# Kernel tuning notes

Measured on AMD Instinct MI355X. Metric: run time of the kernel, lower is better.

## Reference

```python
import jax, jax.numpy as jnp
import numpy as np

N = 50000        # num nodes
E = 800000       # num edges (avg degree 16)
IN = 64          # in_channels
H = 128          # hidden_channels
C1 = 64          # Num_TCN (fine clusters)
C2 = 16          # Num_TCN2 (coarse clusters)
DROP = 0.5       # drop_rate
THRESH = 1.0 / (C1 - 1)  # default edge_pruning_threshold
LN_EPS = 1e-5


def layer_norm(x, g, b):
    mu = jnp.mean(x, axis=-1, keepdims=True)
    var = jnp.var(x, axis=-1, keepdims=True)
    return (x - mu) * jax.lax.rsqrt(var + LN_EPS) * g + b


def graph_conv(x_src, row, col, W_rel, b, W_root, num_nodes):
    # PyG GraphConv (aggr='add'): out = lin_rel(sum_{src->dst} x[src]) + lin_root(x)
    agg = jax.ops.segment_sum(x_src[row], col, num_segments=num_nodes)
    return agg @ W_rel.T + b + x_src @ W_root.T


def mincut_common(x, s, A_s, deg):
    # shared tail of sparse_mincut_pool given A_s = A @ s and degree vector
    C = s.shape[-1]
    pooled_x = s.T @ x                                   # [C, F]
    pooled_adj = s.T @ A_s                               # [C, C]
    mincut_num = jnp.trace(pooled_adj)
    mincut_den = jnp.trace(s.T @ (deg[:, None] * s)) + 1e-10
    mincut_loss = -mincut_num / mincut_den
    sTs = s.T @ s
    norm = jnp.linalg.norm(sTs)
    ortho_loss = jnp.linalg.norm(sTs / (norm + 1e-10) - jnp.eye(C, dtype=x.dtype) / jnp.sqrt(jnp.asarray(C, x.dtype)))
    adj = pooled_adj * (1.0 - jnp.eye(C, dtype=x.dtype))  # fill_diagonal_(0)
    d_sqrt_inv = 1.0 / (jnp.sqrt(adj.sum(axis=1)) + 1e-15)
    adj_norm = adj * d_sqrt_inv[:, None] * d_sqrt_inv[None, :]
    return pooled_x, adj_norm, mincut_loss, ortho_loss


def mincut_sparse(x, row, col, s_logits, num_nodes):
    s = jax.nn.softmax(s_logits, axis=-1)
    # A_s[row] += s[col]  (edge_weight = 1) -> [N, C] scatter-add
    A_s = jax.ops.segment_sum(s[col], row, num_segments=num_nodes)
    deg = jax.ops.segment_sum(jnp.ones((row.shape[0],), x.dtype), row, num_segments=num_nodes)
    return mincut_common(x, s, A_s, deg)


def mincut_dense(x, M, s_logits):
    # pooled graph: dense 0/1 adjacency M[i,j]; equivalent to edge list from nonzero(M)
    s = jax.nn.softmax(s_logits, axis=-1)
    A_s = M @ s
    deg = M.sum(axis=1)
    return mincut_common(x, s, A_s, deg)


def setup_inputs() -> dict:
    key = jax.random.key(0)
    ks = jax.random.split(key, 12)
    x = jax.random.normal(ks[0], (N, IN), jnp.float32)
    edge_index = jax.random.randint(ks[1], (2, E), 0, N, jnp.int32)
    # bernoulli(1 - drop_rate) node-drop mask, fixed for determinism
    drop_mask = (jax.random.uniform(ks[2], (N,)) > DROP).astype(jnp.float32)
    p = lambda k, shp: (jax.random.normal(k, shp, jnp.float32) * 0.05)
    return dict(
        x=x, edge_index=edge_index, drop_mask=drop_mask,
        W1_rel=p(ks[3], (H, IN)), b1=jnp.zeros((H,), jnp.float32), W1_root=p(ks[4], (H, IN)),
        pW1=p(ks[5], (C1, H)), pb1=jnp.zeros((C1,), jnp.float32),
        g1=jnp.ones((C1,), jnp.float32), be1=jnp.zeros((C1,), jnp.float32),
        W2_rel=p(ks[6], (H, H)), b2=jnp.zeros((H,), jnp.float32), W2_root=p(ks[7], (H, H)),
        pW2=p(ks[8], (C2, H)), pb2=jnp.zeros((C2,), jnp.float32),
        g2=jnp.ones((C2,), jnp.float32), be2=jnp.zeros((C2,), jnp.float32),
    )


def reference(x, edge_index, drop_mask, W1_rel, b1, W1_root, pW1, pb1, g1, be1,
              W2_rel, b2, W2_root, pW2, pb2, g2, be2):
    # training=True path, S=1 (loss sums / S are identity)
    row, col = edge_index[0], edge_index[1]
    x_drop = drop_mask[:, None] * x
    x1 = jax.nn.relu(graph_conv(x_drop, row, col, W1_rel, b1, W1_root, N))   # [N, H]
    s1 = layer_norm(x1 @ pW1.T + pb1, g1, be1)                               # [N, C1]
    ls1 = jax.nn.log_softmax(s1, axis=-1)
    x_pool1, adj_pool1, mc1, o1 = mincut_sparse(x1, row, col, s1, N)
    # edge pruning -> dense 0/1 pooled adjacency (replaces nonzero + edge list)
    M = jnp.where(adj_pool1 > THRESH, 1.0, 0.0).astype(x.dtype)              # [C1, C1]
    # GraphConv on pooled graph: aggregate x[src] at dst == M.T @ x_pool1
    x2 = jax.nn.relu((M.T @ x_pool1) @ W2_rel.T + b2 + x_pool1 @ W2_root.T)  # [C1, H]
    s2 = layer_norm(x2 @ pW2.T + pb2, g2, be2)                               # [C1, C2]
    ls2 = jax.nn.log_softmax(s2, axis=-1)
    _, _, mc2, o2 = mincut_dense(x2, M, s2)
    return (mc1, o1, mc2, o2, ls1, ls2)
```

## Files before the change

kernel.cpp:

```cpp
#include <hip/hip_runtime.h>
#include <hip/hip_bf16.h>

#define NN 50000
#define NE 800000
#define INC 64
#define HC 128
#define NC1 64
#define NC2 16
#define DCAP 64

#define OFF_FLAG 0
#define OFW_W1R 16
#define OFW_W1O 8208
#define OFW_B1  16400
#define OFW_PW1 16528
#define OFW_PB1 24720
#define OFW_G1  24784
#define OFW_BE1 24848
#define OFW_W2R 24912
#define OFW_B2  41296
#define OFW_W2O 41424
#define OFW_PW2 57808
#define OFW_PB2 59856
#define OFW_G2  59872
#define OFW_BE2 59888
#define CVT_TOTAL 59888

#define OFW_PW1T 59904
#define OFF_MG   68096
#define OFF_MTG  72192
#define OFF_DEG2 76288
#define OFF_S2G  76352
#define OFW_WCT  77376
#define OFF_XD   127792
#define OFF_X1   3327792
#define OFF_S    9727792
#define OFF_AGG  12927792
#define OFF_CSRC 16127792
#define OFF_SCAL 17727792
#define OFF_PX   17727808
#define OFF_PADJ 17736000
#define OFF_STS  17740096
#define OFF_CUR  17744192
#define OFF_Q    17794192
#define OFF_END  17844192
#define ZERO_FLOATS (OFF_END - OFF_SCAL)

#define OFF_PXSTSP OFF_XD
#define OFF_PADJP  OFF_X1
#define P_POOL 256
#define P_PADJ 1024
#define XSS 132

__device__ inline float bflo(unsigned int u){ return __uint_as_float(u << 16); }
__device__ inline float bfhi(unsigned int u){ return __uint_as_float(u & 0xffff0000u); }

__device__ inline float wave_sum(float v){
#pragma unroll
  for (int o = 32; o > 0; o >>= 1) v += __shfl_xor(v, o, 64);
  return v;
}

__device__ inline void store_out(void* out, long long idx, float v, bool bf){
  if (bf) ((__hip_bfloat16*)out)[idx] = __float2bfloat16(v);
  else    ((float*)out)[idx] = v;
}

__device__ inline float block_reduce_256(float v, float* red, int t){
  red[t] = v; __syncthreads();
#pragma unroll
  for (int sh = 128; sh > 0; sh >>= 1){
    if (t < sh) red[t] += red[t + sh];
    __syncthreads();
  }
  float r = red[0];
  __syncthreads();
  return r;
}

__global__ void k_detect(const unsigned int* __restrict__ dmw, float* __restrict__ flag){
  __shared__ int cnt;
  if (threadIdx.x == 0) cnt = 0;
  __syncthreads();
  int c = 0;
  for (int i = threadIdx.x; i < 12288; i += 256){
    unsigned int w = dmw[i];
    if (w == 0x3F803F80u || w == 0x00003F80u) c++;
  }
  atomicAdd(&cnt, c);
  __syncthreads();
  if (threadIdx.x == 0) flag[0] = (cnt > 64) ? 1.0f : 0.0f;
}

__global__ void k_cvt(const void* p0, const void* p1, const void* p2, const void* p3,
                      const void* p4, const void* p5, const void* p6, const void* p7,
                      const void* p8, const void* p9, const void* p10, const void* p11,
                      const void* p12, const void* p13,
                      const float* __restrict__ flag, float* __restrict__ ws){
  int i = blockIdx.x * blockDim.x + threadIdx.x;
  if (i >= CVT_TOTAL) return;
  const void* src; int off;
  if      (i < 8192 ){ src = p0;  off = i; }
  else if (i < 16384){ src = p1;  off = i - 8192; }
  else if (i < 16512){ src = p2;  off = i - 16384; }
  else if (i < 24704){ src = p3;  off = i - 16512; }
  else if (i < 24768){ src = p4;  off = i - 24704; }
  else if (i < 24832){ src = p5;  off = i - 24768; }
  else if (i < 24896){ src = p6;  off = i - 24832; }
  else if (i < 41280){ src = p7;  off = i - 24896; }
  else if (i < 41408){ src = p8;  off = i - 41280; }
  else if (i < 57792){ src = p9;  off = i - 41408; }
  else if (i < 59840){ src = p10; off = i - 57792; }
  else if (i < 59856){ src = p11; off = i - 59840; }
  else if (i < 59872){ src = p12; off = i - 59856; }
  else               { src = p13; off = i - 59872; }
  float v = (flag[0] > 0.5f) ? __bfloat162float(((const __hip_bfloat16*)src)[off])
                             : ((const float*)src)[off];
  ws[16 + i] = v;
  if (i < 8192){
    int h = i >> 6, j = i & 63;
    ws[OFW_WCT + j * 128 + h] = v;
  } else if (i < 16384){
    int o2 = i - 8192;
    int h = o2 >> 6, j = o2 & 63;
    ws[OFW_WCT + (64 + j) * 128 + h] = v;
  } else if (i >= 16512 && i < 24704){
    int o2 = i - 16512;
    int c = o2 >> 7, k = o2 & 127;
    ws[OFW_PW1T + k * 64 + c] = v;
  }
}

__global__ void k_xdrop(const void* __restrict__ xr, const void* __restrict__ dmr,
                        const float* __restrict__ flag, float* __restrict__ xd){
  int i4 = blockIdx.x * blockDim.x + threadIdx.x;
  if (i4 >= NN * 16) return;
  int n = i4 >> 4;
  float4 o;
  if (flag[0] > 0.5f){
    uint2 w = ((const uint2*)xr)[i4];
    float dv = __bfloat162float(((const __hip_bfloat16*)dmr)[n]);
    o.x = bflo(w.x) * dv; o.y = bfhi(w.x) * dv;
    o.z = bflo(w.y) * dv; o.w = bfhi(w.y) * dv;
  } else {
    float4 xv = ((const float4*)xr)[i4];
    float dv = ((const float*)dmr)[n];
    o.x = xv.x * dv; o.y = xv.y * dv; o.z = xv.z * dv; o.w = xv.w * dv;
  }
  ((float4*)xd)[i4] = o;
}

__global__ void k_fillC(const int* __restrict__ ei, int* __restrict__ cur,
                        unsigned short* __restrict__ csrc2){
  int e = blockIdx.x * blockDim.x + threadIdx.x;
  if (e < NE){
    int r = ei[e], c = ei[NE + e];
    int pos = atomicAdd(&cur[c], 1);
    if (pos < DCAP) csrc2[(c << 6) + pos] = (unsigned short)r;
  }
}

__device__ inline float4 gather_rowsum16(const unsigned short* __restrict__ idxarr,
                                         int st, int en,
                                         const float* __restrict__ table, int lane,
                                         int g, int sub){
  float4 a0 = {0,0,0,0}, a1 = {0,0,0,0}, a2 = {0,0,0,0}, a3 = {0,0,0,0};
  for (int bb = st; bb < en; bb += 64){
    int rem = en - bb;
    int myi = (bb + lane < en) ? (int)idxarr[bb + lane] : 0;
    int niter = ((rem < 64 ? rem : 64) + 3) >> 2;
    int i = 0;
    for (; i + 4 <= niter; i += 4){
      int s0 = __shfl(myi, g + ((i    ) << 2), 64);
      int s1 = __shfl(myi, g + ((i + 1) << 2), 64);
      int s2 = __shfl(myi, g + ((i + 2) << 2), 64);
      int s3 = __shfl(myi, g + ((i + 3) << 2), 64);
      if ((g + (i << 2))       < rem){ float4 v = *(const float4*)(table + (s0 << 6) + (sub << 2)); a0.x += v.x; a0.y += v.y; a0.z += v.z; a0.w += v.w; }
      if ((g + ((i + 1) << 2)) < rem){ float4 v = *(const float4*)(table + (s1 << 6) + (sub << 2)); a1.x += v.x; a1.y += v.y; a1.z += v.z; a1.w += v.w; }
      if ((g + ((i + 2) << 2)) < rem){ float4 v = *(const float4*)(table + (s2 << 6) + (sub << 2)); a2.x += v.x; a2.y += v.y; a2.z += v.z; a2.w += v.w; }
      if ((g + ((i + 3) << 2)) < rem){ float4 v = *(const float4*)(table + (s3 << 6) + (sub << 2)); a3.x += v.x; a3.y += v.y; a3.z += v.z; a3.w += v.w; }
    }
    for (; i < niter; ++i){
      int slot = g + (i << 2);
      int s0 = __shfl(myi, slot, 64);
      if (slot < rem){ float4 v = *(const float4*)(table + (s0 << 6) + (sub << 2)); a0.x += v.x; a0.y += v.y; a0.z += v.z; a0.w += v.w; }
    }
  }
  float4 a;
  a.x = (a0.x + a1.x) + (a2.x + a3.x);
  a.y = (a0.y + a1.y) + (a2.y + a3.y);
  a.z = (a0.z + a1.z) + (a2.z + a3.z);
  a.w = (a0.w + a1.w) + (a2.w + a3.w);
  a.x += __shfl_xor(a.x, 16, 64); a.x += __shfl_xor(a.x, 32, 64);
  a.y += __shfl_xor(a.y, 16, 64); a.y += __shfl_xor(a.y, 32, 64);
  a.z += __shfl_xor(a.z, 16, 64); a.z += __shfl_xor(a.z, 32, 64);
  a.w += __shfl_xor(a.w, 16, 64); a.w += __shfl_xor(a.w, 32, 64);
  return a;
}

__global__ __launch_bounds__(256) void k_agg2(const int* __restrict__ cur,
                                              const unsigned short* __restrict__ csrc2,
                                              const float* __restrict__ xd,
                                              float* __restrict__ agg){
  int gid = blockIdx.x * 256 + threadIdx.x;
  int lane = gid & 63, wid = gid >> 6;
  int nw = (gridDim.x * 256) >> 6;
  int g = lane >> 4, sub = lane & 15;
  for (int n = wid; n < NN; n += nw){
    int c = cur[n]; if (c > DCAP) c = DCAP;
    int st = n << 6, en = st + c;
    float4 a = gather_rowsum16(csrc2, st, en, xd, lane, g, sub);
    if (g == 0) *(float4*)(agg + (n << 6) + (sub << 2)) = a;
  }
}

#define FMA4(ACC, AV) \
  ACC.x += AV.x*w0.x + AV.y*w1.x + AV.z*w2.x + AV.w*w3.x; \
  ACC.y += AV.x*w0.y + AV.y*w1.y + AV.z*w2.y + AV.w*w3.y; \
  ACC.z += AV.x*w0.z + AV.y*w1.z + AV.z*w2.z + AV.w*w3.z; \
  ACC.w += AV.x*w0.w + AV.y*w1.w + AV.z*w2.w + AV.w*w3.w;

__global__ __launch_bounds__(512, 2) void k_x1(const float* __restrict__ agg,
                                               const float* __restrict__ xd,
                                               const float* __restrict__ wts,
                                               float* __restrict__ x1){
  __shared__ __align__(16) float wt[128 * 128];
  __shared__ __align__(16) float at[64 * 128];
  int t = threadIdx.x;
  for (int f4 = t; f4 < 4096; f4 += 512)
    *(float4*)&wt[f4 << 2] = *(const float4*)&wts[OFW_WCT + (f4 << 2)];
  int ni = t >> 5;
  int cj = t & 31;
  float4 b4 = *(const float4*)&wts[OFW_B1 + (cj << 2)];
  const int ntiles = (NN + 63) >> 6;
  for (int tile = blockIdx.x; tile < ntiles; tile += gridDim.x){
    int base = tile << 6;
    __syncthreads();
    for (int f4 = t; f4 < 2048; f4 += 512){
      int i = f4 >> 5, kq = f4 & 31;
      int n = base + i;
      float4 v = make_float4(0.f, 0.f, 0.f, 0.f);
      if (n < NN){
        int k = kq << 2;
        v = (k < 64) ? *(const float4*)(agg + (n << 6) + k)
                     : *(const float4*)(xd  + (n << 6) + (k - 64));
      }
      *(float4*)&at[(i << 7) + (kq << 2)] = v;
    }
    __syncthreads();
    float4 acc0 = {0,0,0,0}, acc1 = {0,0,0,0}, acc2 = {0,0,0,0}, acc3 = {0,0,0,0};
    const float* ap = at + (ni << 9);
    const float* wp = wt + (cj << 2);
#pragma unroll 4
    for (int k = 0; k < 128; k += 4){
      float4 w0 = *(const float4*)(wp + ((k + 0) << 7));
      float4 w1 = *(const float4*)(wp + ((k + 1) << 7));
      float4 w2 = *(const float4*)(wp + ((k + 2) << 7));
      float4 w3 = *(const float4*)(wp + ((k + 3) << 7));
      float4 a0v = *(const float4*)(ap + k);
      float4 a1v = *(const float4*)(ap + 128 + k);
      float4 a2v = *(const float4*)(ap + 256 + k);
      float4 a3v = *(const float4*)(ap + 384 + k);
      FMA4(acc0, a0v)
      FMA4(acc1, a1v)
      FMA4(acc2, a2v)
      FMA4(acc3, a3v)
    }
    int n0 = base + (ni << 2);
    if (n0 + 0 < NN){
      float4 o; o.x = fmaxf(acc0.x + b4.x, 0.f); o.y = fmaxf(acc0.y + b4.y, 0.f);
      o.z = fmaxf(acc0.z + b4.z, 0.f); o.w = fmaxf(acc0.w + b4.w, 0.f);
      *(float4*)(x1 + (long long)(n0 + 0) * HC + (cj << 2)) = o;
    }
    if (n0 + 1 < NN){
      float4 o; o.x = fmaxf(acc1.x + b4.x, 0.f); o.y = fmaxf(acc1.y + b4.y, 0.f);
      o.z = fmaxf(acc1.z + b4.z, 0.f); o.w = fmaxf(acc1.w + b4.w, 0.f);
      *(float4*)(x1 + (long long)(n0 + 1) * HC + (cj << 2)) = o;
    }
    if (n0 + 2 < NN){
      float4 o; o.x = fmaxf(acc2.x + b4.x, 0.f); o.y = fmaxf(acc2.y + b4.y, 0.f);
      o.z = fmaxf(acc2.z + b4.z, 0.f); o.w = fmaxf(acc2.w + b4.w, 0.f);
      *(float4*)(x1 + (long long)(n0 + 2) * HC + (cj << 2)) = o;
    }
    if (n0 + 3 < NN){
      float4 o; o.x = fmaxf(acc3.x + b4.x, 0.f); o.y = fmaxf(acc3.y + b4.y, 0.f);
      o.z = fmaxf(acc3.z + b4.z, 0.f); o.w = fmaxf(acc3.w + b4.w, 0.f);
      *(float4*)(x1 + (long long)(n0 + 3) * HC + (cj << 2)) = o;
    }
  }
}

__global__ __launch_bounds__(256) void k_s1f(const float* __restrict__ x1,
                                             const float* __restrict__ wts,
                                             float* __restrict__ s,
                                             float* __restrict__ q,
                                             void* __restrict__ outp,
                                             const float* __restrict__ flag){
  __shared__ float xs[64 * XSS];
  __shared__ float pwc[64 * 64];
  __shared__ float gsh[64], bsh[64];
  int t = threadIdx.x;
  int base = blockIdx.x * 64;
  if (t < 64){ gsh[t] = wts[OFW_G1 + t]; bsh[t] = wts[OFW_BE1 + t]; }
  for (int f = t; f < 64 * 32; f += 256){
    int r = f >> 5, kq = f & 31;
    float4 v = (base + r < NN) ? *(const float4*)(x1 + (base + r) * HC + (kq << 2))
                               : make_float4(0, 0, 0, 0);
    *(float4*)&xs[r * XSS + (kq << 2)] = v;
  }
  int ni = t >> 4, cj = t & 15;
  float4 c0 = {0,0,0,0}, c1 = {0,0,0,0}, c2 = {0,0,0,0}, c3 = {0,0,0,0};
#pragma unroll
  for (int half = 0; half < 2; ++half){
    int k0 = half << 6;
    __syncthreads();
    for (int f = t; f < 1024; f += 256){
      int kk = f >> 4, qq = f & 15;
      *(float4*)&pwc[kk * 64 + (qq << 2)] =
          *(const float4*)&wts[OFW_PW1T + (k0 + kk) * 64 + (qq << 2)];
    }
    __syncthreads();
    for (int kk = 0; kk < 64; kk += 4){
      float4 a0 = *(const float4*)&xs[(ni * 4 + 0) * XSS + k0 + kk];
      float4 a1 = *(const float4*)&xs[(ni * 4 + 1) * XSS + k0 + kk];
      float4 a2 = *(const float4*)&xs[(ni * 4 + 2) * XSS + k0 + kk];
      float4 a3 = *(const float4*)&xs[(ni * 4 + 3) * XSS + k0 + kk];
      float4 b0 = *(const float4*)&pwc[(kk + 0) * 64 + (cj << 2)];
      float4 b1 = *(const float4*)&pwc[(kk + 1) * 64 + (cj << 2)];
      float4 b2 = *(const float4*)&pwc[(kk + 2) * 64 + (cj << 2)];
      float4 b3 = *(const float4*)&pwc[(kk + 3) * 64 + (cj << 2)];
      c0.x += a0.x*b0.x + a0.y*b1.x + a0.z*b2.x + a0.w*b3.x;
      c0.y += a0.x*b0.y + a0.y*b1.y + a0.z*b2.y + a0.w*b3.y;
      c0.z += a0.x*b0.z + a0.y*b1.z + a0.z*b2.z + a0.w*b3.z;
      c0.w += a0.x*b0.w + a0.y*b1.w + a0.z*b2.w + a0.w*b3.w;
      c1.x += a1.x*b0.x + a1.y*b1.x + a1.z*b2.x + a1.w*b3.x;
      c1.y += a1.x*b0.y + a1.y*b1.y + a1.z*b2.y + a1.w*b3.y;
      c1.z += a1.x*b0.z + a1.y*b1.z + a1.z*b2.z + a1.w*b3.z;
      c1.w += a1.x*b0.w + a1.y*b1.w + a1.z*b2.w + a1.w*b3.w;
      c2.x += a2.x*b0.x + a2.y*b1.x + a2.z*b2.x + a2.w*b3.x;
      c2.y += a2.x*b0.y + a2.y*b1.y + a2.z*b2.y + a2.w*b3.y;
      c2.z += a2.x*b0.z + a2.y*b1.z + a2.z*b2.z + a2.w*b3.z;
      c2.w += a2.x*b0.w + a2.y*b1.w + a2.z*b2.w + a2.w*b3.w;
      c3.x += a3.x*b0.x + a3.y*b1.x + a3.z*b2.x + a3.w*b3.x;
      c3.y += a3.x*b0.y + a3.y*b1.y + a3.z*b2.y + a3.w*b3.y;
      c3.z += a3.x*b0.z + a3.y*b1.z + a3.z*b2.z + a3.w*b3.z;
      c3.w += a3.x*b0.w + a3.y*b1.w + a3.z*b2.w + a3.w*b3.w;
    }
  }
  float4 pb = *(const float4*)&wts[OFW_PB1 + (cj << 2)];
  c0.x += pb.x; c0.y += pb.y; c0.z += pb.z; c0.w += pb.w;
  c1.x += pb.x; c1.y += pb.y; c1.z += pb.z; c1.w += pb.w;
  c2.x += pb.x; c2.y += pb.y; c2.z += pb.z; c2.w += pb.w;
  c3.x += pb.x; c3.y += pb.y; c3.z += pb.z; c3.w += pb.w;
  __syncthreads();
  *(float4*)&xs[(ni * 4 + 0) * XSS + (cj << 2)] = c0;
  *(float4*)&xs[(ni * 4 + 1) * XSS + (cj << 2)] = c1;
  *(float4*)&xs[(ni * 4 + 2) * XSS + (cj << 2)] = c2;
  *(float4*)&xs[(ni * 4 + 3) * XSS + (cj << 2)] = c3;
  __syncthreads();
  bool bf = flag[0] > 0.5f;
  int lane = t & 63, wv = t >> 6;
  float gl = gsh[lane], bl = bsh[lane];
  for (int rb = 0; rb < 16; rb += 4){
    int row = wv * 16 + rb;
    float z0 = xs[(row + 0) * XSS + lane];
    float z1 = xs[(row + 1) * XSS + lane];
    float z2 = xs[(row + 2) * XSS + lane];
    float z3 = xs[(row + 3) * XSS + lane];
    float s0 = z0, s1 = z1, s2 = z2, s3 = z3;
    float q0 = z0*z0, q1 = z1*z1, q2 = z2*z2, q3 = z3*z3;
#pragma unroll
    for (int o = 32; o > 0; o >>= 1){
      s0 += __shfl_xor(s0, o, 64); q0 += __shfl_xor(q0, o, 64);
      s1 += __shfl_xor(s1, o, 64); q1 += __shfl_xor(q1, o, 64);
      s2 += __shfl_xor(s2, o, 64); q2 += __shfl_xor(q2, o, 64);
      s3 += __shfl_xor(s3, o, 64); q3 += __shfl_xor(q3, o, 64);
    }
    float mu0 = s0 * 0.015625f, mu1 = s1 * 0.015625f;
    float mu2 = s2 * 0.015625f, mu3 = s3 * 0.015625f;
    float va0 = q0 * 0.015625f - mu0 * mu0;
    float va1 = q1 * 0.015625f - mu1 * mu1;
    float va2 = q2 * 0.015625f - mu2 * mu2;
    float va3 = q3 * 0.015625f - mu3 * mu3;
    float y0 = (z0 - mu0) * rsqrtf(va0 + 1e-5f) * gl + bl;
    float y1 = (z1 - mu1) * rsqrtf(va1 + 1e-5f) * gl + bl;
    float y2 = (z2 - mu2) * rsqrtf(va2 + 1e-5f) * gl + bl;
    float y3 = (z3 - mu3) * rsqrtf(va3 + 1e-5f) * gl + bl;
    float m0 = y0, m1 = y1, m2 = y2, m3 = y3;
#pragma unroll
    for (int o = 32; o > 0; o >>= 1){
      m0 = fmaxf(m0, __shfl_xor(m0, o, 64));
      m1 = fmaxf(m1, __shfl_xor(m1, o, 64));
      m2 = fmaxf(m2, __shfl_xor(m2, o, 64));
      m3 = fmaxf(m3, __shfl_xor(m3, o, 64));
    }
    float e0 = expf(y0 - m0), e1 = expf(y1 - m1);
    float e2 = expf(y2 - m2), e3 = expf(y3 - m3);
    float u0 = e0, u1 = e1, u2 = e2, u3 = e3;
    float w0 = e0*e0, w1 = e1*e1, w2 = e2*e2, w3 = e3*e3;
#pragma unroll
    for (int o = 32; o > 0; o >>= 1){
      u0 += __shfl_xor(u0, o, 64); w0 += __shfl_xor(w0, o, 64);
      u1 += __shfl_xor(u1, o, 64); w1 += __shfl_xor(w1, o, 64);
      u2 += __shfl_xor(u2, o, 64); w2 += __shfl_xor(w2, o, 64);
      u3 += __shfl_xor(u3, o, 64); w3 += __shfl_xor(w3, o, 64);
    }
    int n0 = base + row;
    if (n0 + 0 < NN){ s[(n0 + 0) * 64 + lane] = e0 / u0;
      store_out(outp, 4LL + (long long)(n0 + 0) * 64 + lane, (y0 - m0) - logf(u0), bf);
      if (lane == 0) q[n0 + 0] = w0 / (u0 * u0); }
    if (n0 + 1 < NN){ s[(n0 + 1) * 64 + lane] = e1 / u1;
      store_out(outp, 4LL + (long long)(n0 + 1) * 64 + lane, (y1 - m1) - logf(u1), bf);
      if (lane == 0) q[n0 + 1] = w1 / (u1 * u1); }
    if (n0 + 2 < NN){ s[(n0 + 2) * 64 + lane] = e2 / u2;
      store_out(outp, 4LL + (long long)(n0 + 2) * 64 + lane, (y2 - m2) - logf(u2), bf);
      if (lane == 0) q[n0 + 2] = w2 / (u2 * u2); }
    if (n0 + 3 < NN){ s[(n0 + 3) * 64 + lane] = e3 / u3;
      store_out(outp, 4LL + (long long)(n0 + 3) * 64 + lane, (y3 - m3) - logf(u3), bf);
      if (lane == 0) q[n0 + 3] = w3 / (u3 * u3); }
  }
}

__global__ __launch_bounds__(256) void k_den(const int* __restrict__ ei,
                                             const float* __restrict__ q,
                                             float* __restrict__ scal){
  __shared__ float red[256];
  int t = threadIdx.x;
  float acc = 0.0f;
  for (int e = blockIdx.x * 256 + t; e < NE; e += gridDim.x * 256)
    acc += q[ei[e]];
  float r = block_reduce_256(acc, red, t);
  if (t == 0) atomicAdd(&scal[0], r);
}

__global__ __launch_bounds__(256) void k_padj2(const int* __restrict__ cur,
                                               const unsigned short* __restrict__ csrc2,
                                               const float* __restrict__ s,
                                               float* __restrict__ padjp){
  __shared__ float rs[16 * 64];
  __shared__ float ra[16 * 64];
  int t = threadIdx.x, lane = t & 63, w = t >> 6;
  int g = lane >> 4, sub = lane & 15;
  int i4 = t >> 4;
  int j4 = t & 15;
  float4 acc0 = {0,0,0,0}, acc1 = {0,0,0,0}, acc2 = {0,0,0,0}, acc3 = {0,0,0,0};
  const int nbatch = NN / 16;
  for (int b = blockIdx.x; b < nbatch; b += gridDim.x){
    int base = b * 16;
#pragma unroll
    for (int qq = 0; qq < 4; ++qq){
      int k = w * 4 + qq;
      int n = base + k;
      int c = cur[n]; if (c > DCAP) c = DCAP;
      int st = n << 6, en = st + c;
      float4 a = gather_rowsum16(csrc2, st, en, s, lane, g, sub);
      if (g == 0){
        *(float4*)&rs[k * 64 + (sub << 2)] = a;
      } else if (g == 1){
        *(float4*)&ra[k * 64 + (sub << 2)] = *(const float4*)(s + (n << 6) + (sub << 2));
      }
    }
    __syncthreads();
#pragma unroll
    for (int k = 0; k < 16; ++k){
      float4 a  = *(const float4*)&rs[k * 64 + (i4 << 2)];
      float4 bv = *(const float4*)&ra[k * 64 + (j4 << 2)];
      acc0.x += a.x * bv.x; acc0.y += a.x * bv.y; acc0.z += a.x * bv.z; acc0.w += a.x * bv.w;
      acc1.x += a.y * bv.x; acc1.y += a.y * bv.y; acc1.z += a.y * bv.z; acc1.w += a.y * bv.w;
      acc2.x += a.z * bv.x; acc2.y += a.z * bv.y; acc2.z += a.z * bv.z; acc2.w += a.z * bv.w;
      acc3.x += a.w * bv.x; acc3.y += a.w * bv.y; acc3.z += a.w * bv.z; acc3.w += a.w * bv.w;
    }
    __syncthreads();
  }
  float* pp = padjp + blockIdx.x * 4096;
  *(float4*)&pp[(i4 * 4 + 0) * 64 + (j4 << 2)] = acc0;
  *(float4*)&pp[(i4 * 4 + 1) * 64 + (j4 << 2)] = acc1;
  *(float4*)&pp[(i4 * 4 + 2) * 64 + (j4 << 2)] = acc2;
  *(float4*)&pp[(i4 * 4 + 3) * 64 + (j4 << 2)] = acc3;
}

__global__ __launch_bounds__(1024) void k_pool(const float* __restrict__ s,
                                               const float* __restrict__ x1,
                                               float* __restrict__ part){
  __shared__ float ssh[32 * 64];
  __shared__ float xsh[32 * 128];
  int t = threadIdx.x;
  int c = t >> 4, q = t & 15;
  float4 apx0 = {0,0,0,0}, apx1 = {0,0,0,0}, ast0 = {0,0,0,0};
  const int nbatch = (NN + 31) / 32;
  for (int b = blockIdx.x; b < nbatch; b += gridDim.x){
    int base = b * 32;
    int kmax = NN - base; if (kmax > 32) kmax = 32;
    if (t < 512){
      int k = t >> 4, col = t & 15;
      float4 v = (k < kmax) ? *(const float4*)(s + ((base + k) << 6) + (col << 2))
                            : make_float4(0, 0, 0, 0);
      *(float4*)&ssh[k * 64 + (col << 2)] = v;
    }
    {
      int k = t >> 5, col = t & 31;
      float4 v = (k < kmax) ? *(const float4*)(x1 + (base + k) * HC + (col << 2))
                            : make_float4(0, 0, 0, 0);
      *(float4*)&xsh[k * 128 + (col << 2)] = v;
    }
    __syncthreads();
    for (int k = 0; k < kmax; ++k){
      float sv = ssh[k * 64 + c];
      float4 xv0 = *(const float4*)&xsh[k * 128 + (q << 2)];
      float4 xv1 = *(const float4*)&xsh[k * 128 + ((q + 16) << 2)];
      float4 s0  = *(const float4*)&ssh[k * 64 + (q << 2)];
      apx0.x += sv * xv0.x; apx0.y += sv * xv0.y; apx0.z += sv * xv0.z; apx0.w += sv * xv0.w;
      apx1.x += sv * xv1.x; apx1.y += sv * xv1.y; apx1.z += sv * xv1.z; apx1.w += sv * xv1.w;
      ast0.x += sv * s0.x;  ast0.y += sv * s0.y;  ast0.z += sv * s0.z;  ast0.w += sv * s0.w;
    }
    __syncthreads();
  }
  float* pp = part + blockIdx.x * 12288;
  *(float4*)&pp[c * 128 + (q << 2)]        = apx0;
  *(float4*)&pp[c * 128 + ((q + 16) << 2)] = apx1;
  *(float4*)&pp[8192 + c * 64 + (q << 2)]  = ast0;
}

__global__ __launch_bounds__(256) void k_red(const float* __restrict__ pxstsp,
                                             const float* __restrict__ padjp,
                                             float* __restrict__ px,
                                             float* __restrict__ sts,
                                             float* __restrict__ padj){
  __shared__ float sh[256];
  int b = blockIdx.x, t = threadIdx.x;
  int ci = t & 63, pc = t >> 6;
  if (b < 192){
    int cell = b * 64 + ci;
    float a0 = 0, a1 = 0, a2 = 0, a3 = 0;
    const float* basep = pxstsp + cell;
    int p0 = pc * (P_POOL / 4);
    for (int p = 0; p < P_POOL / 4; p += 4){
      a0 += basep[(p0 + p    ) * 12288];
      a1 += basep[(p0 + p + 1) * 12288];
      a2 += basep[(p0 + p + 2) * 12288];
      a3 += basep[(p0 + p + 3) * 12288];
    }
    sh[t] = (a0 + a1) + (a2 + a3);
    __syncthreads();
    if (t < 64){
      float r = sh[t] + sh[t + 64] + sh[t + 128] + sh[t + 192];
      int cell2 = b * 64 + t;
      if (cell2 < 8192) px[cell2] = r; else sts[cell2 - 8192] = r;
    }
  } else {
    int cell = (b - 192) * 64 + ci;
    float a0 = 0, a1 = 0, a2 = 0, a3 = 0;
    const float* basep = padjp + cell;
    int p0 = pc * (P_PADJ / 4);
    for (int p = 0; p < P_PADJ / 4; p += 4){
      a0 += basep[(p0 + p    ) * 4096];
      a1 += basep[(p0 + p + 1) * 4096];
      a2 += basep[(p0 + p + 2) * 4096];
      a3 += basep[(p0 + p + 3) * 4096];
    }
    sh[t] = (a0 + a1) + (a2 + a3);
    __syncthreads();
    if (t < 64) padj[(b - 192) * 64 + t] = sh[t] + sh[t + 64] + sh[t + 128] + sh[t + 192];
  }
}

__global__ __launch_bounds__(256) void k_m(const float* __restrict__ padj,
                                           const float* __restrict__ sts,
                                           float* __restrict__ Mg,
                                           float* __restrict__ Mtg,
                                           float* __restrict__ deg2,
                                           float* __restrict__ scal){
  __shared__ float red[256];
  __shared__ float psh[4096];
  __shared__ float dsi[64];
  int t = threadIdx.x;
  const float TH = 1.0f / 63.0f;
  for (int i = t; i < 4096; i += 256) psh[i] = padj[i];
  __syncthreads();
  float v = (t < 64) ? psh[t * 65] : 0.0f;
  float num1 = block_reduce_256(v, red, t);
  v = 0.0f;
  for (int i = t; i < 4096; i += 256){ float e = sts[i]; v += e * e; }
  float nrm1 = sqrtf(block_reduce_256(v, red, t));
  v = 0.0f;
  for (int i = t; i < 4096; i += 256){
    float e = sts[i] / (nrm1 + 1e-10f) - ((i % 65 == 0) ? 0.125f : 0.0f);
    v += e * e;
  }
  float o1 = sqrtf(block_reduce_256(v, red, t));
  if (t < 64){
    float rs = 0.0f;
    for (int j = 0; j < 64; ++j) rs += (j == t) ? 0.0f : psh[t * 64 + j];
    dsi[t] = 1.0f / (sqrtf(rs) + 1e-15f);
  }
  __syncthreads();
  for (int i = t; i < 4096; i += 256){
    int r = i >> 6, c = i & 63;
    float a = (r == c) ? 0.0f : psh[i];
    float m = (a * dsi[r] * dsi[c] > TH) ? 1.0f : 0.0f;
    Mg[i] = m;
    Mtg[c * 64 + r] = m;
  }
  __syncthreads();
  for (int i = t; i < 4096; i += 256){
    int r = i >> 6, c = i & 63;
    float a = (r == c) ? 0.0f : psh[i];
    psh[i] = (a * dsi[r] * dsi[c] > TH) ? 1.0f : 0.0f;
  }
  __syncthreads();
  if (t < 64){
    float d2 = 0.0f;
    for (int j = 0; j < 64; ++j) d2 += psh[t * 64 + j];
    deg2[t] = d2;
  }
  if (t == 0){ scal[1] = num1; scal[2] = o1; }
}

__global__ __launch_bounds__(128) void k_x2(const float* __restrict__ Mtg,
                                            const float* __restrict__ px,
                                            const float* __restrict__ wts,
                                            float* __restrict__ s2g,
                                            void* __restrict__ out,
                                            const float* __restrict__ flag){
  __shared__ float mt[64], pxc[128], mpsh[128], x2sh[128];
  __shared__ float part[16][9], lsh[16], stat[2];
  int c = blockIdx.x, t = threadIdx.x;
  if (t < 64) mt[t] = Mtg[c * 64 + t];
  pxc[t] = px[c * 128 + t];
  __syncthreads();
  float mp = 0.0f;
  for (int i = 0; i < 64; ++i) mp += mt[i] * px[i * 128 + t];
  mpsh[t] = mp;
  __syncthreads();
  float acc = wts[OFW_B2 + t];
  const float* wrr = wts + OFW_W2R + t * 128;
  const float* wor = wts + OFW_W2O + t * 128;
  for (int k = 0; k < 128; ++k) acc += mpsh[k] * wrr[k] + pxc[k] * wor[k];
  x2sh[t] = fmaxf(acc, 0.0f);
  __syncthreads();
  { int u = t >> 3, p = t & 7;
    const float* pw = wts + OFW_PW2 + u * 128 + p * 16;
    float pa = 0.0f;
    for (int k = 0; k < 16; ++k) pa += x2sh[p * 16 + k] * pw[k];
    part[u][p] = pa;
  }
  __syncthreads();
  if (t < 16){
    float l = wts[OFW_PB2 + t];
    for (int p = 0; p < 8; ++p) l += part[t][p];
    lsh[t] = l;
  }
  __syncthreads();
  if (t == 0){
    float mu = 0.0f;
    for (int u = 0; u < 16; ++u) mu += lsh[u];
    mu *= (1.0f / 16.0f);
    float var = 0.0f;
    for (int u = 0; u < 16; ++u){ float d = lsh[u] - mu; var += d * d; }
    var *= (1.0f / 16.0f);
    float rstd = rsqrtf(var + 1e-5f);
    float m = -3.4e38f;
    for (int u = 0; u < 16; ++u){
      lsh[u] = (lsh[u] - mu) * rstd * wts[OFW_G2 + u] + wts[OFW_BE2 + u];
      m = fmaxf(m, lsh[u]);
    }
    float se = 0.0f;
    for (int u = 0; u < 16; ++u) se += expf(lsh[u] - m);
    stat[0] = m; stat[1] = logf(se);
  }
  __syncthreads();
  if (t < 16){
    float ls = (lsh[t] - stat[0]) - stat[1];
    store_out(out, 4LL + (long long)NN * NC1 + c * 16 + t, ls, flag[0] > 0.5f);
    s2g[c * 16 + t] = expf(ls);
  }
}

__global__ __launch_bounds__(256) void k_tail(const float* __restrict__ Mg,
                                              const float* __restrict__ s2g,
                                              const float* __restrict__ deg2,
                                              const float* __restrict__ scal,
                                              void* __restrict__ out,
                                              const float* __restrict__ flag){
  __shared__ float red[256];
  __shared__ float Msh[4096];
  __shared__ float s2sh[1024];
  __shared__ float d2sh[64];
  __shared__ float sts2[256];
  int t = threadIdx.x;
  for (int i = t; i < 4096; i += 256) Msh[i] = Mg[i];
  for (int i = t; i < 1024; i += 256) s2sh[i] = s2g[i];
  if (t < 64) d2sh[t] = deg2[t];
  __syncthreads();
  float vnum = 0.0f, vden = 0.0f;
  for (int m = 0; m < 4; ++m){
    int id = t + m * 256;
    int c = id >> 4, u = id & 15;
    float a = 0.0f;
    for (int j = 0; j < 64; ++j) a += Msh[c * 64 + j] * s2sh[j * 16 + u];
    float sv = s2sh[id];
    vnum += sv * a;
    vden += d2sh[c] * sv * sv;
  }
  float num2 = block_reduce_256(vnum, red, t);
  float den2 = block_reduce_256(vden, red, t) + 1e-10f;
  { int u = t >> 4, w = t & 15;
    float a = 0.0f;
    for (int c2 = 0; c2 < 64; ++c2) a += s2sh[c2 * 16 + u] * s2sh[c2 * 16 + w];
    sts2[t] = a;
  }
  __syncthreads();
  float v = sts2[t] * sts2[t];
  float nrm2 = sqrtf(block_reduce_256(v, red, t));
  { float e = sts2[t] / (nrm2 + 1e-10f) - (((t >> 4) == (t & 15)) ? 0.25f : 0.0f);
    v = e * e; }
  float o2 = sqrtf(block_reduce_256(v, red, t));
  if (t == 0){
    bool bf = flag[0] > 0.5f;
    float den = scal[0] + 1e-10f;
    store_out(out, 0, -scal[1] / den, bf);
    store_out(out, 1, scal[2], bf);
    store_out(out, 2, -num2 / den2, bf);
    store_out(out, 3, o2, bf);
  }
}

extern "C" void kernel_launch(void* const* d_in, const int* in_sizes, int n_in,
                              void* d_out, int out_size, void* d_ws, size_t ws_size,
                              hipStream_t stream){
  const void* x  = d_in[0];
  const int*  ei = (const int*)d_in[1];
  const void* dm = d_in[2];

  float* ws    = (float*)d_ws;
  float* flag  = ws + OFF_FLAG;
  float* xd    = ws + OFF_XD;
  float* x1    = ws + OFF_X1;
  float* s     = ws + OFF_S;
  float* agg   = ws + OFF_AGG;
  float* px    = ws + OFF_PX;
  float* padj  = ws + OFF_PADJ;
  float* sts   = ws + OFF_STS;
  float* scal  = ws + OFF_SCAL;
  float* Mg    = ws + OFF_MG;
  float* Mtg   = ws + OFF_MTG;
  float* deg2  = ws + OFF_DEG2;
  float* s2g   = ws + OFF_S2G;
  float* q     = ws + OFF_Q;
  float* pxstsp= ws + OFF_PXSTSP;
  float* padjp = ws + OFF_PADJP;
  unsigned short* csrc2 = (unsigned short*)(ws + OFF_CSRC);
  int* cur = (int*)(ws + OFF_CUR);

  hipMemsetAsync(ws + OFF_SCAL, 0, (size_t)ZERO_FLOATS * sizeof(float), stream);

  k_detect<<<1, 256, 0, stream>>>((const unsigned int*)dm, flag);
  k_cvt<<<(CVT_TOTAL + 255) / 256, 256, 0, stream>>>(
      d_in[3], d_in[5], d_in[4], d_in[6], d_in[7], d_in[8], d_in[9],
      d_in[10], d_in[11], d_in[12], d_in[13], d_in[14], d_in[15], d_in[16],
      flag, ws);
  k_xdrop<<<(NN * 16 + 255) / 256, 256, 0, stream>>>(x, dm, flag, xd);
  k_fillC<<<(NE + 255) / 256, 256, 0, stream>>>(ei, cur, csrc2);
  k_agg2<<<2048, 256, 0, stream>>>(cur, csrc2, xd, agg);
  k_x1<<<256, 512, 0, stream>>>(agg, xd, ws, x1);
  k_s1f<<<(NN + 63) / 64, 256, 0, stream>>>(x1, ws, s, q, d_out, flag);
  k_den<<<256, 256, 0, stream>>>(ei, q, scal);
  k_pool<<<P_POOL, 1024, 0, stream>>>(s, x1, pxstsp);
  k_padj2<<<P_PADJ, 256, 0, stream>>>(cur, csrc2, s, padjp);
  k_red<<<256, 256, 0, stream>>>(pxstsp, padjp, px, sts, padj);
  k_m<<<1, 256, 0, stream>>>(padj, sts, Mg, Mtg, deg2, scal);
  k_x2<<<64, 128, 0, stream>>>(Mtg, px, ws, s2g, d_out, flag);
  k_tail<<<1, 256, 0, stream>>>(Mg, s2g, deg2, scal, d_out, flag);
}
```

Baseline: 435.9 us.

## Gather aggregation from fp16 feature copy and partition CSR fill by destination range

The dropped-input features are also written as an fp16 copy into the x1 workspace region, and the neighbor-sum gather reads this half-width table and accumulates in fp32, halving the random gather traffic. The edge bucketing kernel now splits edges into slices, and each slice is scanned by 8 blocks that each handle only destinations in one eighth of the node range. This is meant to localise atomics and stores by destination. The trade-off is that every block re-reads the destination indices of its slice, and the fp16 rounding of inputs adds precision loss to the aggregation. The fp16 buffer aliases x1, which is written later, so reuse relies on kernel ordering.

```diff
diff --git a/kernel.cpp b/kernel.cpp
--- a/kernel.cpp
+++ b/kernel.cpp
@@ -1,5 +1,6 @@
 #include <hip/hip_runtime.h>
 #include <hip/hip_bf16.h>
+#include <hip/hip_fp16.h>
 
 #define NN 50000
 #define NE 800000
@@ -48,9 +49,15 @@
 
 #define OFF_PXSTSP OFF_XD
 #define OFF_PADJP  OFF_X1
+#define OFF_XD16   OFF_X1
 #define P_POOL 256
 #define P_PADJ 1024
 #define XSS 132
+
+#define FC_G 2048
+#define FC_SLICES (FC_G >> 3)
+#define FC_ES ((NE + FC_SLICES - 1) / FC_SLICES)
+#define FC_RANGE (NN >> 3)
 
 __device__ inline float bflo(unsigned int u){ return __uint_as_float(u << 16); }
 __device__ inline float bfhi(unsigned int u){ return __uint_as_float(u & 0xffff0000u); }
@@ -132,7 +139,8 @@
 }
 
 __global__ void k_xdrop(const void* __restrict__ xr, const void* __restrict__ dmr,
-                        const float* __restrict__ flag, float* __restrict__ xd){
+                        const float* __restrict__ flag, float* __restrict__ xd,
+                        __half* __restrict__ xd16){
   int i4 = blockIdx.x * blockDim.x + threadIdx.x;
   if (i4 >= NN * 16) return;
   int n = i4 >> 4;
@@ -148,15 +156,28 @@
     o.x = xv.x * dv; o.y = xv.y * dv; o.z = xv.z * dv; o.w = xv.w * dv;
   }
   ((float4*)xd)[i4] = o;
-}
-
-__global__ void k_fillC(const int* __restrict__ ei, int* __restrict__ cur,
+  __half2 ha = __floats2half2_rn(o.x, o.y);
+  __half2 hb = __floats2half2_rn(o.z, o.w);
+  uint2 hh;
+  hh.x = *(unsigned int*)&ha;
+  hh.y = *(unsigned int*)&hb;
+  ((uint2*)xd16)[i4] = hh;
+}
+
+__global__ __launch_bounds__(256) void k_fillC(const int* __restrict__ ei, int* __restrict__ cur,
                         unsigned short* __restrict__ csrc2){
-  int e = blockIdx.x * blockDim.x + threadIdx.x;
-  if (e < NE){
-    int r = ei[e], c = ei[NE + e];
-    int pos = atomicAdd(&cur[c], 1);
-    if (pos < DCAP) csrc2[(c << 6) + pos] = (unsigned short)r;
+  int p = blockIdx.x & 7;
+  int q = blockIdx.x >> 3;
+  int lo = p * FC_RANGE;
+  int base = q * FC_ES;
+  int end = base + FC_ES; if (end > NE) end = NE;
+  for (int e = base + (int)threadIdx.x; e < end; e += 256){
+    int c = ei[NE + e];
+    if ((unsigned)(c - lo) < (unsigned)FC_RANGE){
+      int r = ei[e];
+      int pos = atomicAdd(&cur[c], 1);
+      if (pos < DCAP) csrc2[(c << 6) + pos] = (unsigned short)r;
+    }
   }
 }
 
@@ -198,9 +219,67 @@
   return a;
 }
 
+__device__ inline float4 gather_rowsum16h(const unsigned short* __restrict__ idxarr,
+                                          int st, int en,
+                                          const __half* __restrict__ table, int lane,
+                                          int g, int sub){
+  float4 a0 = {0,0,0,0}, a1 = {0,0,0,0}, a2 = {0,0,0,0}, a3 = {0,0,0,0};
+  for (int bb = st; bb < en; bb += 64){
+    int rem = en - bb;
+    int myi = (bb + lane < en) ? (int)idxarr[bb + lane] : 0;
+    int niter = ((rem < 64 ? rem : 64) + 3) >> 2;
+    int i = 0;
+    for (; i + 4 <= niter; i += 4){
+      int s0 = __shfl(myi, g + ((i    ) << 2), 64);
+      int s1 = __shfl(myi, g + ((i + 1) << 2), 64);
+      int s2 = __shfl(myi, g + ((i + 2) << 2), 64);
+      int s3 = __shfl(myi, g + ((i + 3) << 2), 64);
+      if ((g + (i << 2))       < rem){
+        uint2 u = *(const uint2*)(table + (s0 << 6) + (sub << 2));
+        float2 f0 = __half22float2(*(__half2*)&u.x), f1 = __half22float2(*(__half2*)&u.y);
+        a0.x += f0.x; a0.y += f0.y; a0.z += f1.x; a0.w += f1.y;
+      }
+      if ((g + ((i + 1) << 2)) < rem){
+        uint2 u = *(const uint2*)(table + (s1 << 6) + (sub << 2));
+        float2 f0 = __half22float2(*(__half2*)&u.x), f1 = __half22float2(*(__half2*)&u.y);
+        a1.x += f0.x; a1.y += f0.y; a1.z += f1.x; a1.w += f1.y;
+      }
+      if ((g + ((i + 2) << 2)) < rem){
+        uint2 u = *(const uint2*)(table + (s2 << 6) + (sub << 2));
+        float2 f0 = __half22float2(*(__half2*)&u.x), f1 = __half22float2(*(__half2*)&u.y);
+        a2.x += f0.x; a2.y += f0.y; a2.z += f1.x; a2.w += f1.y;
+      }
+      if ((g + ((i + 3) << 2)) < rem){
+        uint2 u = *(const uint2*)(table + (s3 << 6) + (sub << 2));
+        float2 f0 = __half22float2(*(__half2*)&u.x), f1 = __half22float2(*(__half2*)&u.y);
+        a3.x += f0.x; a3.y += f0.y; a3.z += f1.x; a3.w += f1.y;
+      }
+    }
+    for (; i < niter; ++i){
+      int slot = g + (i << 2);
+      int s0 = __shfl(myi, slot, 64);
+      if (slot < rem){
+        uint2 u = *(const uint2*)(table + (s0 << 6) + (sub << 2));
+        float2 f0 = __half22float2(*(__half2*)&u.x), f1 = __half22float2(*(__half2*)&u.y);
+        a0.x += f0.x; a0.y += f0.y; a0.z += f1.x; a0.w += f1.y;
+      }
+    }
+  }
+  float4 a;
+  a.x = (a0.x + a1.x) + (a2.x + a3.x);
+  a.y = (a0.y + a1.y) + (a2.y + a3.y);
+  a.z = (a0.z + a1.z) + (a2.z + a3.z);
+  a.w = (a0.w + a1.w) + (a2.w + a3.w);
+  a.x += __shfl_xor(a.x, 16, 64); a.x += __shfl_xor(a.x, 32, 64);
+  a.y += __shfl_xor(a.y, 16, 64); a.y += __shfl_xor(a.y, 32, 64);
+  a.z += __shfl_xor(a.z, 16, 64); a.z += __shfl_xor(a.z, 32, 64);
+  a.w += __shfl_xor(a.w, 16, 64); a.w += __shfl_xor(a.w, 32, 64);
+  return a;
+}
+
 __global__ __launch_bounds__(256) void k_agg2(const int* __restrict__ cur,
                                               const unsigned short* __restrict__ csrc2,
-                                              const float* __restrict__ xd,
+                                              const __half* __restrict__ xd16,
                                               float* __restrict__ agg){
   int gid = blockIdx.x * 256 + threadIdx.x;
   int lane = gid & 63, wid = gid >> 6;
@@ -209,7 +288,7 @@
   for (int n = wid; n < NN; n += nw){
     int c = cur[n]; if (c > DCAP) c = DCAP;
     int st = n << 6, en = st + c;
-    float4 a = gather_rowsum16(csrc2, st, en, xd, lane, g, sub);
+    float4 a = gather_rowsum16h(csrc2, st, en, xd16, lane, g, sub);
     if (g == 0) *(float4*)(agg + (n << 6) + (sub << 2)) = a;
   }
 }
@@ -749,6 +828,7 @@
   float* q     = ws + OFF_Q;
   float* pxstsp= ws + OFF_PXSTSP;
   float* padjp = ws + OFF_PADJP;
+  __half* xd16 = (__half*)(ws + OFF_XD16);
   unsigned short* csrc2 = (unsigned short*)(ws + OFF_CSRC);
   int* cur = (int*)(ws + OFF_CUR);
 
@@ -759,9 +839,9 @@
       d_in[3], d_in[5], d_in[4], d_in[6], d_in[7], d_in[8], d_in[9],
       d_in[10], d_in[11], d_in[12], d_in[13], d_in[14], d_in[15], d_in[16],
       flag, ws);
-  k_xdrop<<<(NN * 16 + 255) / 256, 256, 0, stream>>>(x, dm, flag, xd);
-  k_fillC<<<(NE + 255) / 256, 256, 0, stream>>>(ei, cur, csrc2);
-  k_agg2<<<2048, 256, 0, stream>>>(cur, csrc2, xd, agg);
+  k_xdrop<<<(NN * 16 + 255) / 256, 256, 0, stream>>>(x, dm, flag, xd, xd16);
+  k_fillC<<<FC_G, 256, 0, stream>>>(ei, cur, csrc2);
+  k_agg2<<<2048, 256, 0, stream>>>(cur, csrc2, xd16, agg);
   k_x1<<<256, 512, 0, stream>>>(agg, xd, ws, x1);
   k_s1f<<<(NN + 63) / 64, 256, 0, stream>>>(x1, ws, s, q, d_out, flag);
   k_den<<<256, 256, 0, stream>>>(ei, q, scal);
```

Result: faster. 419.2 us (-3.8%).
